# Kernel optimization log

Hardware: AMD Instinct MI355X
Metric: run time of the kernel (lower is better)

The kernel has to match this reference:

```python
import jax, jax.numpy as jnp
import numpy as np

D_MODEL = 512
NHEAD = 8


def setup_inputs() -> dict:
    key = jax.random.key(0)
    k0, k1, k2 = jax.random.split(key, 3)
    s = 1.0 / np.sqrt(D_MODEL)  # torch default uniform init bound (xavier-ish)
    return {
        "x": jax.random.normal(k0, (2, 4096, D_MODEL), dtype=jnp.float32),
        "in_proj_w": jax.random.uniform(k1, (3 * D_MODEL, D_MODEL), jnp.float32, -s, s),
        "in_proj_b": jnp.zeros((3 * D_MODEL,), jnp.float32),
        "out_proj_w": jax.random.uniform(k2, (D_MODEL, D_MODEL), jnp.float32, -s, s),
        "out_proj_b": jnp.zeros((D_MODEL,), jnp.float32),
        "window_size": 128,
    }


def reference(x, in_proj_w, in_proj_b, out_proj_w, out_proj_b, window_size):
    # Faithful to nn.MultiheadAttention (eval mode, dropout inactive).
    # NOTE: PyTorch bool attn_mask: True = disallowed. The module sets True
    # INSIDE the window, so in-window positions are masked OUT.
    B, S, D = x.shape
    H = NHEAD
    hd = D // H

    qkv = x @ in_proj_w.T + in_proj_b                      # [B,S,3D]
    q, k, v = jnp.split(qkv, 3, axis=-1)
    q = q.reshape(B, S, H, hd).transpose(0, 2, 1, 3)       # [B,H,S,hd]
    k = k.reshape(B, S, H, hd).transpose(0, 2, 1, 3)
    v = v.reshape(B, S, H, hd).transpose(0, 2, 1, 3)

    scores = jnp.einsum('bhqd,bhkd->bhqk', q, k) / jnp.sqrt(jnp.float32(hd))

    idx = jnp.arange(S)
    in_window = jnp.abs(idx[:, None] - idx[None, :]) <= window_size  # [S,S]
    scores = jnp.where(in_window, -jnp.inf, scores)

    attn = jax.nn.softmax(scores, axis=-1)                 # [B,H,S,S]
    ctx = jnp.einsum('bhqk,bhkd->bhqd', attn, v)           # [B,H,S,hd]
    ctx = ctx.transpose(0, 2, 1, 3).reshape(B, S, D)       # [B,S,D]
    return ctx @ out_proj_w.T + out_proj_b
```

## Files before the change

kernel.cpp:

```cpp
#include <hip/hip_runtime.h>
#include <hip/hip_bf16.h>

typedef unsigned short u16;
typedef __bf16 bf16x8 __attribute__((ext_vector_type(8)));
typedef short s16x4 __attribute__((ext_vector_type(4)));
typedef float f32x4 __attribute__((ext_vector_type(4)));

__device__ __forceinline__ f32x4 mfma16(bf16x8 a, bf16x8 b, f32x4 c) {
    return __builtin_amdgcn_mfma_f32_16x16x32_bf16(a, b, c, 0, 0, 0);
}
__device__ __forceinline__ f32x4 mfma16k16(s16x4 a, s16x4 b, f32x4 c) {
    return __builtin_amdgcn_mfma_f32_16x16x16bf16_1k(a, b, c, 0, 0, 0);
}

__device__ __forceinline__ u16 f2b(float x) {
    union { float f; unsigned u; } a; a.f = x;
    unsigned r = a.u + 0x7fffu + ((a.u >> 16) & 1u);
    return (u16)(r >> 16);
}
__device__ __forceinline__ unsigned f2b2(float a, float b) {
    union { __hip_bfloat162 h; unsigned u; } cv;
    cv.h = __float22bfloat162_rn(make_float2(a, b));
    return cv.u;
}

#define NX  (8192 * 512)
#define NWQ (1536 * 512)
#define NWO (512 * 512)
__global__ __launch_bounds__(256) void k_cast_all(const float* __restrict__ x,
                                                  const float* __restrict__ wq,
                                                  const float* __restrict__ wo,
                                                  u16* __restrict__ xb,
                                                  u16* __restrict__ wqb,
                                                  u16* __restrict__ wob) {
    int i = (blockIdx.x * 256 + threadIdx.x) * 4;
    const float* s; u16* d; int off;
    if (i < NX)            { s = x;  d = xb;  off = i; }
    else if (i < NX + NWQ) { s = wq; d = wqb; off = i - NX; }
    else                   { s = wo; d = wob; off = i - NX - NWQ; }
    float4 f = *(const float4*)&s[off];
    uint2 o = make_uint2(f2b2(f.x, f.y), f2b2(f.z, f.w));
    *(uint2*)&d[off] = o;
}

__global__ __launch_bounds__(256) void k_gemm_qkv(const u16* __restrict__ xb,
                                                  const u16* __restrict__ wb,
                                                  const float* __restrict__ bias,
                                                  u16* __restrict__ qkvout) {
    __shared__ u16 As[128][40];
    __shared__ u16 Ws[128][40];
    const int tid = threadIdx.x;
    const int w = tid >> 6, lane = tid & 63, l15 = lane & 15, quad = lane >> 4;
    const int mb = blockIdx.x * 128, nb = blockIdx.y * 128;

    f32x4 acc[2][8];
#pragma unroll
    for (int i = 0; i < 2; i++)
#pragma unroll
        for (int j = 0; j < 8; j++) acc[i][j] = (f32x4){0.f, 0.f, 0.f, 0.f};

    for (int k0 = 0; k0 < 512; k0 += 32) {
        {
            int row = tid >> 1, cc = (tid & 1) * 16;
            const u16* g = &xb[(size_t)(mb + row) * 512 + k0 + cc];
            *(uint4*)&As[row][cc]     = *(const uint4*)g;
            *(uint4*)&As[row][cc + 8] = *(const uint4*)(g + 8);
            const u16* gw = &wb[(size_t)(nb + row) * 512 + k0 + cc];
            *(uint4*)&Ws[row][cc]     = *(const uint4*)gw;
            *(uint4*)&Ws[row][cc + 8] = *(const uint4*)(gw + 8);
        }
        __syncthreads();
        bf16x8 a0 = *(const bf16x8*)&As[w * 32 + l15][quad * 8];
        bf16x8 a1 = *(const bf16x8*)&As[w * 32 + 16 + l15][quad * 8];
#pragma unroll
        for (int nt = 0; nt < 8; nt++) {
            bf16x8 bfr = *(const bf16x8*)&Ws[nt * 16 + l15][quad * 8];
            acc[0][nt] = mfma16(a0, bfr, acc[0][nt]);
            acc[1][nt] = mfma16(a1, bfr, acc[1][nt]);
        }
        __syncthreads();
    }
    const int seg = nb >> 9;
    u16* obase = qkvout + (size_t)seg * (16ull * 4096 * 64);
    if (seg < 2) {
        const float sc = (seg == 0) ? 0.125f * 1.44269504088896340736f : 1.0f;
#pragma unroll
        for (int mt = 0; mt < 2; mt++)
#pragma unroll
            for (int nt = 0; nt < 8; nt++) {
                int dcol = nb + nt * 16 + l15;
                int hh = (dcol >> 6) & 7, dloc = dcol & 63;
                float bs = bias[dcol];
#pragma unroll
                for (int r = 0; r < 4; r++) {
                    int m = mb + w * 32 + mt * 16 + quad * 4 + r;
                    float vv = (acc[mt][nt][r] + bs) * sc;
                    int b = m >> 12, s = m & 4095;
                    obase[((size_t)((b * 8 + hh) * 4096 + s)) * 64 + dloc] = f2b(vv);
                }
            }
    } else {
#pragma unroll
        for (int mt = 0; mt < 2; mt++)
#pragma unroll
            for (int nt = 0; nt < 8; nt++) {
                int c = nb + nt * 16 + l15;
                int hh = (c >> 6) & 7, d = c & 63;
                int mbv = d >> 4, l15v = d & 15;
                float bs = bias[c];
                int m0 = mb + w * 32 + mt * 16 + quad * 4;
                int b = m0 >> 12, si = m0 & 4095;
                int kt = si >> 6, ka = si & 63;
                int ntv = ka >> 4;
                uint2 o = make_uint2(f2b2(acc[mt][nt][0] + bs, acc[mt][nt][1] + bs),
                                     f2b2(acc[mt][nt][2] + bs, acc[mt][nt][3] + bs));
                size_t F4 = ((((((size_t)(b * 8 + hh) * 64 + kt) * 4 + ntv) * 4 + mbv) * 4 + quad) * 16 + l15v);
                *(uint2*)&obase[F4 * 4] = o;
            }
    }
}

__global__ __launch_bounds__(128, 2) void k_attn(const u16* __restrict__ qkv,
                                                 const u16* __restrict__ vfg,
                                                 u16* __restrict__ ctx,
                                                 const int* __restrict__ win) {
    __shared__ u16 Ks[2][64][64];
    const int tid = threadIdx.x;
    const int w = tid >> 6, lane = tid & 63, l15 = lane & 15, quad = lane >> 4;
    const int bh = blockIdx.y;
    const int qb0 = blockIdx.x * 64;
    const int W = win[0];
    const u16* qg = qkv;
    const u16* kg = qkv + 16ull * 4096 * 64;
    const size_t bhb = (size_t)bh * 4096 * 64;

    bf16x8 qf[2][2];
#pragma unroll
    for (int g = 0; g < 2; g++) {
        const u16* qrow = &qg[bhb + (size_t)(qb0 + w * 32 + g * 16 + l15) * 64];
        qf[g][0] = *(const bf16x8*)&qrow[quad * 8];
        qf[g][1] = *(const bf16x8*)&qrow[32 + quad * 8];
    }

    f32x4 O[2][4];
#pragma unroll
    for (int g = 0; g < 2; g++)
#pragma unroll
        for (int mb = 0; mb < 4; mb++) O[g][mb] = (f32x4){0.f, 0.f, 0.f, 0.f};
    float lsum[2] = {0.f, 0.f};

    const int srow = tid >> 1, half = tid & 1, sw = srow & 7;
    const u16* kgr = &kg[bhb + (size_t)srow * 64 + half * 32];
    const u16* vb0 = vfg + (size_t)bh * 64 * 4096 + lane * 4;

    int it = 0;
    for (int kb = 0; kb < 4096; kb += 64) {
        if (max(qb0 + 63 - kb, kb + 63 - qb0) <= W) continue;
        bool partial = (kb + 63 >= qb0 - W) && (kb <= qb0 + 63 + W);
        int p = it & 1; it++;
        const u16* vt0 = vb0 + (size_t)(kb >> 6) * 4096;
        const u16* vt1 = vt0 + 2048;
        s16x4 vfr[16];
#pragma unroll
        for (int f = 0; f < 8; f++) vfr[f]     = *(const s16x4*)&vt0[f * 256];
#pragma unroll
        for (int f = 0; f < 8; f++) vfr[f + 8] = *(const s16x4*)&vt1[f * 256];
        {
            const u16* kp = kgr + (size_t)kb * 64;
            uint4 kr0 = *(const uint4*)kp;
            uint4 kr1 = *(const uint4*)(kp + 8);
            uint4 kr2 = *(const uint4*)(kp + 16);
            uint4 kr3 = *(const uint4*)(kp + 24);
            int cb = half * 4;
            *(uint4*)&Ks[p][srow][((cb + 0) ^ sw) * 8] = kr0;
            *(uint4*)&Ks[p][srow][((cb + 1) ^ sw) * 8] = kr1;
            *(uint4*)&Ks[p][srow][((cb + 2) ^ sw) * 8] = kr2;
            *(uint4*)&Ks[p][srow][((cb + 3) ^ sw) * 8] = kr3;
        }
        __syncthreads();
        bf16x8 kf[4][2];
        const int rs = l15 & 7;
#pragma unroll
        for (int nt = 0; nt < 4; nt++) {
            kf[nt][0] = *(const bf16x8*)&Ks[p][nt * 16 + l15][(quad ^ rs) * 8];
            kf[nt][1] = *(const bf16x8*)&Ks[p][nt * 16 + l15][((quad + 4) ^ rs) * 8];
        }
#pragma unroll
        for (int g = 0; g < 2; g++) {
            f32x4 C[4];
#pragma unroll
            for (int nt = 0; nt < 4; nt++) {
                f32x4 z = (f32x4){0.f, 0.f, 0.f, 0.f};
                C[nt] = mfma16(kf[nt][0], qf[g][0], z);
                C[nt] = mfma16(kf[nt][1], qf[g][1], C[nt]);
            }
            s16x4 pb[4];
            if (!partial) {
#pragma unroll
                for (int nt = 0; nt < 4; nt++) {
                    float p0 = __builtin_amdgcn_exp2f(C[nt][0]);
                    float p1 = __builtin_amdgcn_exp2f(C[nt][1]);
                    float p2 = __builtin_amdgcn_exp2f(C[nt][2]);
                    float p3 = __builtin_amdgcn_exp2f(C[nt][3]);
                    lsum[g] += (p0 + p1) + (p2 + p3);
                    union { uint2 u; s16x4 v; } pk;
                    pk.u = make_uint2(f2b2(p0, p1), f2b2(p2, p3));
                    pb[nt] = pk.v;
                }
            } else {
                int qr = qb0 + w * 32 + g * 16 + l15;
#pragma unroll
                for (int nt = 0; nt < 4; nt++) {
                    float pv[4];
#pragma unroll
                    for (int r = 0; r < 4; r++) {
                        int key = kb + nt * 16 + quad * 4 + r;
                        int dd = qr - key; dd = dd < 0 ? -dd : dd;
                        pv[r] = (dd <= W) ? 0.f : __builtin_amdgcn_exp2f(C[nt][r]);
                        lsum[g] += pv[r];
                    }
                    union { uint2 u; s16x4 v; } pk;
                    pk.u = make_uint2(f2b2(pv[0], pv[1]), f2b2(pv[2], pv[3]));
                    pb[nt] = pk.v;
                }
            }
#pragma unroll
            for (int nt = 0; nt < 4; nt++)
#pragma unroll
                for (int mb = 0; mb < 4; mb++)
                    O[g][mb] = mfma16k16(vfr[nt * 4 + mb], pb[nt], O[g][mb]);
        }
    }
#pragma unroll
    for (int g = 0; g < 2; g++) {
        lsum[g] += __shfl_xor(lsum[g], 16);
        lsum[g] += __shfl_xor(lsum[g], 32);
    }
    int b = bh >> 3, h = bh & 7;
#pragma unroll
    for (int g = 0; g < 2; g++) {
        float inv = 1.0f / lsum[g];
        int qr = qb0 + w * 32 + g * 16 + l15;
        size_t rowoff = ((size_t)(b * 4096 + qr)) * 512 + h * 64;
#pragma unroll
        for (int mb = 0; mb < 4; mb++) {
            uint2 o = make_uint2(f2b2(O[g][mb][0] * inv, O[g][mb][1] * inv),
                                 f2b2(O[g][mb][2] * inv, O[g][mb][3] * inv));
            *(uint2*)&ctx[rowoff + mb * 16 + quad * 4] = o;
        }
    }
}

__global__ __launch_bounds__(256) void k_gemm_out(const u16* __restrict__ ab,
                                                  const u16* __restrict__ wb,
                                                  const float* __restrict__ bias,
                                                  float* __restrict__ out) {
    __shared__ u16 As[128][40];
    __shared__ u16 Ws[64][40];
    const int tid = threadIdx.x;
    const int w = tid >> 6, lane = tid & 63, l15 = lane & 15, quad = lane >> 4;
    const int mb = blockIdx.x * 128, nb = blockIdx.y * 64;

    f32x4 acc[2][4];
#pragma unroll
    for (int i = 0; i < 2; i++)
#pragma unroll
        for (int j = 0; j < 4; j++) acc[i][j] = (f32x4){0.f, 0.f, 0.f, 0.f};

    for (int k0 = 0; k0 < 512; k0 += 32) {
        {
            int row = tid >> 1, cc = (tid & 1) * 16;
            const u16* g = &ab[(size_t)(mb + row) * 512 + k0 + cc];
            *(uint4*)&As[row][cc]     = *(const uint4*)g;
            *(uint4*)&As[row][cc + 8] = *(const uint4*)(g + 8);
            int wrow = tid >> 2, wcc = (tid & 3) * 8;
            *(uint4*)&Ws[wrow][wcc] = *(const uint4*)&wb[(size_t)(nb + wrow) * 512 + k0 + wcc];
        }
        __syncthreads();
        bf16x8 a0 = *(const bf16x8*)&As[w * 32 + l15][quad * 8];
        bf16x8 a1 = *(const bf16x8*)&As[w * 32 + 16 + l15][quad * 8];
#pragma unroll
        for (int nt = 0; nt < 4; nt++) {
            bf16x8 bfr = *(const bf16x8*)&Ws[nt * 16 + l15][quad * 8];
            acc[0][nt] = mfma16(a0, bfr, acc[0][nt]);
            acc[1][nt] = mfma16(a1, bfr, acc[1][nt]);
        }
        __syncthreads();
    }
#pragma unroll
    for (int mt = 0; mt < 2; mt++)
#pragma unroll
        for (int nt = 0; nt < 4; nt++) {
            int n = nb + nt * 16 + l15;
            float bs = bias[n];
#pragma unroll
            for (int r = 0; r < 4; r++) {
                int m = mb + w * 32 + mt * 16 + quad * 4 + r;
                out[(size_t)m * 512 + n] = acc[mt][nt][r] + bs;
            }
        }
}

extern "C" void kernel_launch(void* const* d_in, const int* in_sizes, int n_in,
                              void* d_out, int out_size, void* d_ws, size_t ws_size,
                              hipStream_t stream) {
    const float* x    = (const float*)d_in[0];
    const float* wqkv = (const float*)d_in[1];
    const float* bqkv = (const float*)d_in[2];
    const float* wout = (const float*)d_in[3];
    const float* bout = (const float*)d_in[4];
    const int*   win  = (const int*)d_in[5];
    float* out = (float*)d_out;

    u16* xb    = (u16*)d_ws;
    u16* wqkvb = xb    + 8192ull * 512;
    u16* woutb = wqkvb + 1536ull * 512;
    u16* qkvb  = woutb + 512ull * 512;
    u16* ctxb  = qkvb  + 3ull * 16 * 4096 * 64;

    k_cast_all<<<5120, 256, 0, stream>>>(x, wqkv, wout, xb, wqkvb, woutb);
    k_gemm_qkv<<<dim3(64, 12), 256, 0, stream>>>(xb, wqkvb, bqkv, qkvb);
    k_attn<<<dim3(64, 16), 128, 0, stream>>>(qkvb, qkvb + 32ull * 4096 * 64, ctxb, win);
    k_gemm_out<<<dim3(64, 8), 256, 0, stream>>>(ctxb, woutb, bout, out);
}
```

Measured before the change: 241.4 us.

## Load K fragments directly from global per wave and compute row sums via MFMA

The attention kernel drops the shared-memory K staging and the __syncthreads. Each wave now reads its K fragments straight from global memory, and waves run independently, each with its own 32-row query block. Row sums are accumulated by an extra MFMA against a ones vector instead of scalar adds followed by cross-lane shuffles. The block grows to 256 threads with half the grid. K is re-read from global or cache by every wave, and each wave skips key blocks independently, which removes barrier coupling at the cost of more global traffic.

```diff
diff --git a/kernel.cpp b/kernel.cpp
--- a/kernel.cpp
+++ b/kernel.cpp
@@ -120,15 +120,14 @@
     }
 }
 
-__global__ __launch_bounds__(128, 2) void k_attn(const u16* __restrict__ qkv,
-                                                 const u16* __restrict__ vfg,
-                                                 u16* __restrict__ ctx,
-                                                 const int* __restrict__ win) {
-    __shared__ u16 Ks[2][64][64];
+__global__ __launch_bounds__(256) void k_attn(const u16* __restrict__ qkv,
+                                              const u16* __restrict__ vfg,
+                                              u16* __restrict__ ctx,
+                                              const int* __restrict__ win) {
     const int tid = threadIdx.x;
     const int w = tid >> 6, lane = tid & 63, l15 = lane & 15, quad = lane >> 4;
     const int bh = blockIdx.y;
-    const int qb0 = blockIdx.x * 64;
+    const int qb0 = blockIdx.x * 128 + w * 32;
     const int W = win[0];
     const u16* qg = qkv;
     const u16* kg = qkv + 16ull * 4096 * 64;
@@ -137,54 +136,47 @@
     bf16x8 qf[2][2];
 #pragma unroll
     for (int g = 0; g < 2; g++) {
-        const u16* qrow = &qg[bhb + (size_t)(qb0 + w * 32 + g * 16 + l15) * 64];
+        const u16* qrow = &qg[bhb + (size_t)(qb0 + g * 16 + l15) * 64];
         qf[g][0] = *(const bf16x8*)&qrow[quad * 8];
         qf[g][1] = *(const bf16x8*)&qrow[32 + quad * 8];
     }
 
+    const short one_bf = (short)0x3F80;
+    s16x4 onesA;
+    {
+        short v = (l15 == 0) ? one_bf : (short)0;
+        onesA[0] = v; onesA[1] = v; onesA[2] = v; onesA[3] = v;
+    }
+
     f32x4 O[2][4];
 #pragma unroll
     for (int g = 0; g < 2; g++)
 #pragma unroll
         for (int mb = 0; mb < 4; mb++) O[g][mb] = (f32x4){0.f, 0.f, 0.f, 0.f};
-    float lsum[2] = {0.f, 0.f};
-
-    const int srow = tid >> 1, half = tid & 1, sw = srow & 7;
-    const u16* kgr = &kg[bhb + (size_t)srow * 64 + half * 32];
-    const u16* vb0 = vfg + (size_t)bh * 64 * 4096 + lane * 4;
-
-    int it = 0;
+    f32x4 O1[2] = {(f32x4){0.f, 0.f, 0.f, 0.f}, (f32x4){0.f, 0.f, 0.f, 0.f}};
+
+    const u16* klp = &kg[bhb + (size_t)l15 * 64 + quad * 8];
+    const u16* vbl = vfg + (size_t)bh * 64 * 4096 + lane * 4;
+
     for (int kb = 0; kb < 4096; kb += 64) {
         if (max(qb0 + 63 - kb, kb + 63 - qb0) <= W) continue;
         bool partial = (kb + 63 >= qb0 - W) && (kb <= qb0 + 63 + W);
-        int p = it & 1; it++;
-        const u16* vt0 = vb0 + (size_t)(kb >> 6) * 4096;
-        const u16* vt1 = vt0 + 2048;
+
+        const u16* kl = klp + (size_t)kb * 64;
+        bf16x8 kf[4][2];
+#pragma unroll
+        for (int nt = 0; nt < 4; nt++) {
+            kf[nt][0] = *(const bf16x8*)(kl + nt * 1024);
+            kf[nt][1] = *(const bf16x8*)(kl + nt * 1024 + 32);
+        }
+        const u16* vl0 = vbl + (size_t)(kb >> 6) * 4096;
+        const u16* vl1 = vl0 + 2048;
         s16x4 vfr[16];
 #pragma unroll
-        for (int f = 0; f < 8; f++) vfr[f]     = *(const s16x4*)&vt0[f * 256];
-#pragma unroll
-        for (int f = 0; f < 8; f++) vfr[f + 8] = *(const s16x4*)&vt1[f * 256];
-        {
-            const u16* kp = kgr + (size_t)kb * 64;
-            uint4 kr0 = *(const uint4*)kp;
-            uint4 kr1 = *(const uint4*)(kp + 8);
-            uint4 kr2 = *(const uint4*)(kp + 16);
-            uint4 kr3 = *(const uint4*)(kp + 24);
-            int cb = half * 4;
-            *(uint4*)&Ks[p][srow][((cb + 0) ^ sw) * 8] = kr0;
-            *(uint4*)&Ks[p][srow][((cb + 1) ^ sw) * 8] = kr1;
-            *(uint4*)&Ks[p][srow][((cb + 2) ^ sw) * 8] = kr2;
-            *(uint4*)&Ks[p][srow][((cb + 3) ^ sw) * 8] = kr3;
-        }
-        __syncthreads();
-        bf16x8 kf[4][2];
-        const int rs = l15 & 7;
-#pragma unroll
-        for (int nt = 0; nt < 4; nt++) {
-            kf[nt][0] = *(const bf16x8*)&Ks[p][nt * 16 + l15][(quad ^ rs) * 8];
-            kf[nt][1] = *(const bf16x8*)&Ks[p][nt * 16 + l15][((quad + 4) ^ rs) * 8];
-        }
+        for (int f = 0; f < 8; f++) vfr[f]     = *(const s16x4*)(vl0 + f * 256);
+#pragma unroll
+        for (int f = 0; f < 8; f++) vfr[f + 8] = *(const s16x4*)(vl1 + f * 256);
+
 #pragma unroll
         for (int g = 0; g < 2; g++) {
             f32x4 C[4];
@@ -202,13 +194,12 @@
                     float p1 = __builtin_amdgcn_exp2f(C[nt][1]);
                     float p2 = __builtin_amdgcn_exp2f(C[nt][2]);
                     float p3 = __builtin_amdgcn_exp2f(C[nt][3]);
-                    lsum[g] += (p0 + p1) + (p2 + p3);
                     union { uint2 u; s16x4 v; } pk;
                     pk.u = make_uint2(f2b2(p0, p1), f2b2(p2, p3));
                     pb[nt] = pk.v;
                 }
             } else {
-                int qr = qb0 + w * 32 + g * 16 + l15;
+                int qr = qb0 + g * 16 + l15;
 #pragma unroll
                 for (int nt = 0; nt < 4; nt++) {
                     float pv[4];
@@ -217,7 +208,6 @@
                         int key = kb + nt * 16 + quad * 4 + r;
                         int dd = qr - key; dd = dd < 0 ? -dd : dd;
                         pv[r] = (dd <= W) ? 0.f : __builtin_amdgcn_exp2f(C[nt][r]);
-                        lsum[g] += pv[r];
                     }
                     union { uint2 u; s16x4 v; } pk;
                     pk.u = make_uint2(f2b2(pv[0], pv[1]), f2b2(pv[2], pv[3]));
@@ -225,22 +215,20 @@
                 }
             }
 #pragma unroll
-            for (int nt = 0; nt < 4; nt++)
+            for (int nt = 0; nt < 4; nt++) {
 #pragma unroll
                 for (int mb = 0; mb < 4; mb++)
                     O[g][mb] = mfma16k16(vfr[nt * 4 + mb], pb[nt], O[g][mb]);
-        }
-    }
+                O1[g] = mfma16k16(onesA, pb[nt], O1[g]);
+            }
+        }
+    }
+    int b = bh >> 3, h = bh & 7;
 #pragma unroll
     for (int g = 0; g < 2; g++) {
-        lsum[g] += __shfl_xor(lsum[g], 16);
-        lsum[g] += __shfl_xor(lsum[g], 32);
-    }
-    int b = bh >> 3, h = bh & 7;
-#pragma unroll
-    for (int g = 0; g < 2; g++) {
-        float inv = 1.0f / lsum[g];
-        int qr = qb0 + w * 32 + g * 16 + l15;
+        float ls = __shfl(O1[g][0], l15);
+        float inv = 1.0f / ls;
+        int qr = qb0 + g * 16 + l15;
         size_t rowoff = ((size_t)(b * 4096 + qr)) * 512 + h * 64;
 #pragma unroll
         for (int mb = 0; mb < 4; mb++) {
@@ -320,6 +308,6 @@
 
     k_cast_all<<<5120, 256, 0, stream>>>(x, wqkv, wout, xb, wqkvb, woutb);
     k_gemm_qkv<<<dim3(64, 12), 256, 0, stream>>>(xb, wqkvb, bqkv, qkvb);
-    k_attn<<<dim3(64, 16), 128, 0, stream>>>(qkvb, qkvb + 32ull * 4096 * 64, ctxb, win);
+    k_attn<<<dim3(32, 16), 256, 0, stream>>>(qkvb, qkvb + 32ull * 4096 * 64, ctxb, win);
     k_gemm_out<<<dim3(64, 8), 256, 0, stream>>>(ctxb, woutb, bout, out);
 }
```

After: 297.0 us. +23.0%, slower.
